# Optimization experiments

Measured on AMD Instinct MI355X. Metric: run time of the kernel, lower is better.

The kernel has to match this reference:

```python
import jax, jax.numpy as jnp
import numpy as np

B, N, D = 8, 65536, 3
K = 64                 # num_centers
NPOINT = 4096
M = NPOINT // K * 2    # max_neighbors = 128
S = NPOINT // K        # fps samples per group = 64
NITER = 10             # KMeans default Niter


def _sqdist(src, dst):
    # ||s||^2 + ||d||^2 - 2 s.d   (same math as (s-d)^2 sum, GEMM form)
    s2 = (src ** 2).sum(-1)[:, :, None]          # [B,N,1]
    d2 = (dst ** 2).sum(-1)[:, None, :]          # [B,1,K]
    return s2 + d2 - 2.0 * jnp.einsum('bnd,bkd->bnk', src, dst)


def _kmeans(x):
    Bb, Nn, Dd = x.shape
    c = x[:, :K, :]
    bidx = jnp.arange(Bb)[:, None]               # broadcast with cl [B,N]
    for _ in range(NITER):
        cl = jnp.argmin(_sqdist(x, c), axis=2)   # [B,N] cluster codes
        c = jnp.zeros((Bb, K, Dd), x.dtype).at[bidx, cl].add(x)
        ncl = jnp.zeros((Bb, K), x.dtype).at[bidx, cl].add(1.0)
        c = c / ncl[:, :, None]
    return c


def _query_neighbor(x, centers):
    dist = _sqdist(x, centers)                   # [B,N,K]
    negd = -jnp.transpose(dist, (0, 2, 1))       # [B,K,N]
    _, nidx = jax.lax.top_k(negd, M)             # M nearest points per center
    bidx = jnp.arange(x.shape[0])[:, None, None]
    return x[bidx, nidx]                         # [B,K,M,3]


def _batch_fps(xyz, farthest0):
    # xyz: [B,G,Nn,3]; sequential farthest-point sampling per group
    Bb, G, Nn, _ = xyz.shape
    dist0 = jnp.full((Bb, G, Nn), 1e10, xyz.dtype)

    def step(carry, _):
        distance, farthest = carry
        centroid = jnp.take_along_axis(xyz, farthest[:, :, None, None], axis=2)  # [B,G,1,3]
        d = ((xyz - centroid) ** 2).sum(-1)       # [B,G,Nn]
        distance = jnp.minimum(distance, d)
        new_far = jnp.argmax(distance, -1).astype(farthest.dtype)
        return (distance, new_far), farthest      # store index BEFORE update

    _, idx = jax.lax.scan(step, (dist0, farthest0), None, length=S)
    idx = jnp.transpose(idx, (1, 2, 0))           # [B,G,S]
    idx3 = jnp.broadcast_to(idx[..., None], idx.shape + (3,))
    new_xyz = jnp.take_along_axis(xyz, idx3, axis=2)  # [B,G,S,3]
    return new_xyz.reshape(Bb, G * S, 3)


def setup_inputs() -> dict:
    key = jax.random.key(0)
    k1, k2 = jax.random.split(key)
    x = jax.random.normal(k1, (B, N, D), dtype=jnp.float32)
    farthest0 = jax.random.randint(k2, (B, K), 0, M, dtype=jnp.int32)
    return {"x": x, "farthest0": farthest0}


def reference(x, farthest0):
    centers = _kmeans(x)                  # [B,K,3]
    neighbor = _query_neighbor(x, centers)  # [B,K,M,3]
    new_xyz = _batch_fps(neighbor, farthest0)  # [B, NPOINT, 3]
    return new_xyz, centers
```

## Files before the change

### kernel.cpp

```cpp
#include <hip/hip_runtime.h>
#include <stdint.h>

#pragma clang fp contract(off)

#define B 8
#define N 65536
#define KC 64
#define M 128
#define S 64
#define NITER 10
#define TOPK_T 1024
#define NWAVES (TOPK_T / 64)
#define HPAD 257
#define SAMPLE 8192
#define SCAP 2048
#define CAP 2048
#define UPD_T 1024
#define RANGE 16384
#define NRANGE (N / RANGE)
#define PPT (RANGE / UPD_T)
#define GBATCH 2048

using u32 = unsigned int;
using u64 = unsigned long long;

__device__ __forceinline__ float sq3(float a, float b, float c) {
  return __fadd_rn(__fadd_rn(__fmul_rn(a, a), __fmul_rn(b, b)), __fmul_rn(c, c));
}
__device__ __forceinline__ float dot3(float x0, float x1, float x2,
                                      float c0, float c1, float c2) {
  return __fadd_rn(__fadd_rn(__fmul_rn(x0, c0), __fmul_rn(x1, c1)), __fmul_rn(x2, c2));
}
__device__ __forceinline__ float distf(float s2, float d2, float dt) {
  return __fsub_rn(__fadd_rn(s2, d2), __fmul_rn(2.0f, dt));
}
__device__ __forceinline__ u32 fkey(float f) {
  u32 u = __float_as_uint(f);
  return (u & 0x80000000u) ? ~u : (u | 0x80000000u);
}


__global__ void k_init_centers(const float* __restrict__ x, float* __restrict__ centers) {
  int i = blockIdx.x * blockDim.x + threadIdx.x;
  if (i >= B * KC * 3) return;
  int b = i / (KC * 3);
  int r = i % (KC * 3);
  centers[i] = x[(size_t)b * N * 3 + r];
}

__global__ void k_s2(const float* __restrict__ x, float* __restrict__ s2) {
  int i = blockIdx.x * blockDim.x + threadIdx.x;
  const float2* x2 = (const float2*)x;
  float2 A = x2[3 * i], Bv = x2[3 * i + 1], C = x2[3 * i + 2];
  float2 o;
  o.x = sq3(A.x, A.y, Bv.x);
  o.y = sq3(Bv.y, C.x, C.y);
  ((float2*)s2)[i] = o;
}

__global__ void k_assign(const float* __restrict__ x, const float* __restrict__ centers,
                         unsigned char* __restrict__ cl) {
  __shared__ float4 cs[KC];
  int g = blockIdx.x;
  int b = g & 7;
  int chunk = g >> 3;
  int t = threadIdx.x;
  if (t < KC) {
    float a0 = centers[(b * KC + t) * 3 + 0];
    float a1 = centers[(b * KC + t) * 3 + 1];
    float a2 = centers[(b * KC + t) * 3 + 2];
    cs[t] = make_float4(a0, a1, a2, sq3(a0, a1, a2));
  }
  __syncthreads();
  int pr = chunk * 256 + t;
  const float2* xb2 = (const float2*)(x + (size_t)b * N * 3);
  float2 A = xb2[3 * pr], Bv = xb2[3 * pr + 1], C = xb2[3 * pr + 2];
  float s20 = sq3(A.x, A.y, Bv.x);
  float s21 = sq3(Bv.y, C.x, C.y);
  float best0 = __int_as_float(0x7f800000), best1 = best0;
  int bi0 = 0, bi1 = 0;
  for (int k = 0; k < KC; ++k) {
    float4 cc = cs[k];
    float d0 = distf(s20, cc.w, dot3(A.x, A.y, Bv.x, cc.x, cc.y, cc.z));
    float d1 = distf(s21, cc.w, dot3(Bv.y, C.x, C.y, cc.x, cc.y, cc.z));
    if (d0 < best0) { best0 = d0; bi0 = k; }
    if (d1 < best1) { best1 = d1; bi1 = k; }
  }
  *(unsigned short*)(cl + (size_t)b * N + 2 * pr) =
      (unsigned short)(bi0 | (bi1 << 8));
}

__global__ __launch_bounds__(UPD_T)
void k_cluster_update(const float* __restrict__ x, const unsigned char* __restrict__ cl,
                      float* __restrict__ centers) {
  __shared__ unsigned short midx[RANGE];
  __shared__ float bcoord[3][GBATCH + 1];
  __shared__ int woff[NWAVES];
  __shared__ int sCnt;
  int g = blockIdx.x;
  int bk = ((g & 7) << 6) | (g >> 3);
  int b = bk >> 6, k = bk & 63;
  int t = threadIdx.x, lane = t & 63, wid = t >> 6;
  const unsigned char* clb = cl + (size_t)b * N;
  const float* xb = x + (size_t)b * N * 3;
  float acc = 0.f;
  int cntAll = 0;

  for (int r = 0; r < NRANGE; ++r) {
    const uint4* cp = (const uint4*)(clb + r * RANGE);
    uint4 v = cp[t];
    u32 wsv[4] = {v.x, v.y, v.z, v.w};
    int m = 0;
#pragma unroll
    for (int j = 0; j < PPT; ++j)
      m += (((wsv[j >> 2] >> ((j & 3) * 8)) & 255u) == (u32)k);
    int incl = m;
#pragma unroll
    for (int o = 1; o < 64; o <<= 1) {
      int u = __shfl_up(incl, o);
      if (lane >= o) incl += u;
    }
    if (lane == 63) woff[wid] = incl;
    __syncthreads();
    if (t == 0) {
      int run = 0;
      for (int w = 0; w < NWAVES; ++w) { int vv = woff[w]; woff[w] = run; run += vv; }
      sCnt = run;
    }
    __syncthreads();
    int off = woff[wid] + incl - m;
    int mcnt = sCnt;
    int base = t * PPT;
#pragma unroll
    for (int j = 0; j < PPT; ++j) {
      if (((wsv[j >> 2] >> ((j & 3) * 8)) & 255u) == (u32)k)
        midx[off++] = (unsigned short)(base + j);
    }
    __syncthreads();
    for (int bo = 0; bo < mcnt; bo += GBATCH) {
      int bn = min(GBATCH, mcnt - bo);
      for (int i = t; i < bn; i += UPD_T) {
        int li = midx[bo + i];
        size_t src = ((size_t)(r * RANGE + li)) * 3;
        bcoord[0][i] = xb[src];
        bcoord[1][i] = xb[src + 1];
        bcoord[2][i] = xb[src + 2];
      }
      __syncthreads();
      if (wid == 0 && lane < 3) {
        const float* mb = &bcoord[lane][0];
        for (int i = 0; i < bn; ++i) acc = __fadd_rn(acc, mb[i]);
      }
      __syncthreads();
    }
    cntAll += mcnt;
    __syncthreads();
  }
  if (wid == 0 && lane < 3)
    centers[bk * 3 + lane] = __fdiv_rn(acc, (float)cntAll);
}

__global__ __launch_bounds__(TOPK_T)
void k_query_topk(const float* __restrict__ x, const float* __restrict__ s2g,
                  const float* __restrict__ centers, float* __restrict__ neighbor) {
  __shared__ u32 whist[NWAVES * HPAD];
  __shared__ u32 hist[256];
  __shared__ u32 skeys[SCAP];
  __shared__ u64 candList[CAP];
  __shared__ u64 lessList[M];
  __shared__ u32 eqList[256];
  __shared__ u32 sPrefix;
  __shared__ int sNeed, sCntBin;
  __shared__ int cntCand, cntLess, cntEq;
  __shared__ float sc0, sc1, sc2, sd2;

  int g = blockIdx.x;
  int bk = ((g & 7) << 6) | (g >> 3);
  int b = bk >> 6;
  int t = threadIdx.x;
  int wid = t >> 6;
  if (t == 0) {
    float c0 = centers[bk * 3], c1 = centers[bk * 3 + 1], c2 = centers[bk * 3 + 2];
    sc0 = c0; sc1 = c1; sc2 = c2; sd2 = sq3(c0, c1, c2);
    cntCand = 0; cntLess = 0; cntEq = 0;
  }
  for (int i = t; i < NWAVES * HPAD; i += TOPK_T) whist[i] = 0;
  __syncthreads();
  float c0 = sc0, c1 = sc1, c2 = sc2, d2 = sd2;
  const float* xb = x + (size_t)b * N * 3;
  const float2* xb2 = (const float2*)xb;
  const float2* s2b2 = (const float2*)(s2g + (size_t)b * N);

  for (int p = t; p < SAMPLE / 2; p += TOPK_T) {
    float2 A = xb2[3 * p], Bv = xb2[3 * p + 1], C = xb2[3 * p + 2];
    float2 s2p = s2b2[p];
    float d0 = distf(s2p.x, d2, dot3(A.x, A.y, Bv.x, c0, c1, c2));
    float d1 = distf(s2p.y, d2, dot3(Bv.y, C.x, C.y, c0, c1, c2));
    atomicAdd(&whist[wid * HPAD + (fkey(d0) >> 24)], 1u);
    atomicAdd(&whist[wid * HPAD + (fkey(d1) >> 24)], 1u);
  }
  __syncthreads();
  if (t < 256) {
    u32 s = 0;
#pragma unroll
    for (int w = 0; w < NWAVES; ++w) s += whist[w * HPAD + t];
    hist[t] = s;
  }
  __syncthreads();
  if (t == 0) {
    int cum = 0;
    for (int bin = 0; bin < 256; ++bin) {
      int c = (int)hist[bin];
      if (cum + c >= M) { sPrefix = (u32)bin; sNeed = M - cum; sCntBin = c; break; }
      cum += c;
    }
  }
  __syncthreads();
  u32 selByte = sPrefix;
  int needEq = sNeed;
  int cntBin = sCntBin;

  u32 thrK;
  if (cntBin <= SCAP) {
    for (int p = t; p < SAMPLE / 2; p += TOPK_T) {
      float2 A = xb2[3 * p], Bv = xb2[3 * p + 1], C = xb2[3 * p + 2];
      float2 s2p = s2b2[p];
      float d0 = distf(s2p.x, d2, dot3(A.x, A.y, Bv.x, c0, c1, c2));
      float d1 = distf(s2p.y, d2, dot3(Bv.y, C.x, C.y, c0, c1, c2));
      u32 k0 = fkey(d0), k1 = fkey(d1);
      if ((k0 >> 24) == selByte) skeys[atomicAdd(&cntEq, 1)] = k0;
      if ((k1 >> 24) == selByte) skeys[atomicAdd(&cntEq, 1)] = k1;
    }
    __syncthreads();
    int ne = cntEq;
    u32 prefix = selByte << 24;
    int need = needEq;
    for (int sh = 16; sh >= 0; sh -= 8) {
      for (int i = t; i < 256; i += TOPK_T) hist[i] = 0;
      __syncthreads();
      for (int i = t; i < ne; i += TOPK_T) {
        u32 kk = skeys[i];
        if ((kk >> (sh + 8)) == (prefix >> (sh + 8)))
          atomicAdd(&hist[(kk >> sh) & 255u], 1u);
      }
      __syncthreads();
      if (t == 0) {
        int cum = 0;
        for (int bin = 0; bin < 256; ++bin) {
          int c = (int)hist[bin];
          if (cum + c >= need) { sPrefix = prefix | ((u32)bin << sh); sNeed = need - cum; break; }
          cum += c;
        }
      }
      __syncthreads();
      prefix = sPrefix; need = sNeed;
      __syncthreads();
    }
    thrK = prefix;
  } else {
    thrK = (selByte << 24) | 0x00FFFFFFu;
  }

  for (int p = t; p < N / 2; p += TOPK_T) {
    float2 A = xb2[3 * p], Bv = xb2[3 * p + 1], C = xb2[3 * p + 2];
    float2 s2p = s2b2[p];
    float d0 = distf(s2p.x, d2, dot3(A.x, A.y, Bv.x, c0, c1, c2));
    float d1 = distf(s2p.y, d2, dot3(Bv.y, C.x, C.y, c0, c1, c2));
    u32 k0 = fkey(d0), k1 = fkey(d1);
    if (k0 <= thrK) {
      int q = atomicAdd(&cntCand, 1);
      if (q < CAP) candList[q] = ((u64)k0 << 32) | (u32)(2 * p);
    }
    if (k1 <= thrK) {
      int q = atomicAdd(&cntCand, 1);
      if (q < CAP) candList[q] = ((u64)k1 << 32) | (u32)(2 * p + 1);
    }
  }
  __syncthreads();
  int cc = cntCand;

  if (cc <= CAP) {
    int P = 1; while (P < cc) P <<= 1;
    if (P < M) P = M;
    for (int i = t; i < P; i += TOPK_T) if (i >= cc) candList[i] = ~0ull;
    __syncthreads();
    for (int ksz = 2; ksz <= P; ksz <<= 1) {
      for (int j = ksz >> 1; j > 0; j >>= 1) {
        for (int idx = t; idx < P; idx += TOPK_T) {
          int ixj = idx ^ j;
          if (ixj > idx) {
            u64 a = candList[idx], bb = candList[ixj];
            bool up = ((idx & ksz) == 0);
            if (up ? (a > bb) : (a < bb)) { candList[idx] = bb; candList[ixj] = a; }
          }
        }
        __syncthreads();
      }
    }
    if (t < M) {
      int idx = (int)(candList[t] & 0xFFFFFFFFu);
      size_t src = ((size_t)b * N + idx) * 3;
      size_t dst = ((size_t)bk * M + t) * 3;
      neighbor[dst]     = x[src];
      neighbor[dst + 1] = x[src + 1];
      neighbor[dst + 2] = x[src + 2];
    }
    return;
  }

  u32 prefix = 0;
  int need = M;
  for (int r = 3; r >= 0; --r) {
    for (int i = t; i < 256; i += TOPK_T) hist[i] = 0;
    __syncthreads();
    int sh = r * 8;
    for (int n = t; n < N; n += TOPK_T) {
      float x0 = xb[n * 3], x1 = xb[n * 3 + 1], x2 = xb[n * 3 + 2];
      float d = distf(sq3(x0, x1, x2), d2, dot3(x0, x1, x2, c0, c1, c2));
      u32 key = fkey(d);
      bool ok = (r == 3) || ((key >> (sh + 8)) == (prefix >> (sh + 8)));
      if (ok) atomicAdd(&hist[(key >> sh) & 255u], 1u);
    }
    __syncthreads();
    if (t == 0) {
      int cum = 0;
      for (int bin = 0; bin < 256; ++bin) {
        int c = (int)hist[bin];
        if (cum + c >= need) { sPrefix = prefix | ((u32)bin << sh); sNeed = need - cum; break; }
        cum += c;
      }
    }
    __syncthreads();
    prefix = sPrefix; need = sNeed;
    __syncthreads();
  }
  u32 K128 = prefix;

  if (t == 0) { cntLess = 0; cntEq = 0; }
  __syncthreads();
  for (int n = t; n < N; n += TOPK_T) {
    float x0 = xb[n * 3], x1 = xb[n * 3 + 1], x2 = xb[n * 3 + 2];
    float d = distf(sq3(x0, x1, x2), d2, dot3(x0, x1, x2, c0, c1, c2));
    u32 key = fkey(d);
    if (key < K128) {
      int p = atomicAdd(&cntLess, 1);
      if (p < M) lessList[p] = ((u64)key << 32) | (u32)n;
    } else if (key == K128) {
      int p = atomicAdd(&cntEq, 1);
      if (p < 256) eqList[p] = (u32)n;
    }
  }
  __syncthreads();
  int nl = cntLess;
  int ne2 = cntEq;
  for (int i = t; i < M; i += TOPK_T) if (i >= nl) lessList[i] = ~0ull;
  for (int i = t; i < 256; i += TOPK_T) if (i >= ne2) eqList[i] = 0xFFFFFFFFu;
  __syncthreads();

  for (int ksz = 2; ksz <= M; ksz <<= 1) {
    for (int j = ksz >> 1; j > 0; j >>= 1) {
      for (int idx = t; idx < M; idx += TOPK_T) {
        int ixj = idx ^ j;
        if (ixj > idx) {
          u64 a = lessList[idx], bb = lessList[ixj];
          bool up = ((idx & ksz) == 0);
          if (up ? (a > bb) : (a < bb)) { lessList[idx] = bb; lessList[ixj] = a; }
        }
      }
      __syncthreads();
    }
  }
  for (int ksz = 2; ksz <= 256; ksz <<= 1) {
    for (int j = ksz >> 1; j > 0; j >>= 1) {
      for (int idx = t; idx < 256; idx += TOPK_T) {
        int ixj = idx ^ j;
        if (ixj > idx) {
          u32 a = eqList[idx], bb = eqList[ixj];
          bool up = ((idx & ksz) == 0);
          if (up ? (a > bb) : (a < bb)) { eqList[idx] = bb; eqList[ixj] = a; }
        }
      }
      __syncthreads();
    }
  }

  if (t < M) {
    int idx = (t < nl) ? (int)(lessList[t] & 0xFFFFFFFFu) : (int)eqList[t - nl];
    size_t src = ((size_t)b * N + idx) * 3;
    size_t dst = ((size_t)bk * M + t) * 3;
    neighbor[dst]     = x[src];
    neighbor[dst + 1] = x[src + 1];
    neighbor[dst + 2] = x[src + 2];
  }
}

__global__ void k_fps(const float* __restrict__ neighbor, const int* __restrict__ farthest0,
                      const float* __restrict__ centers, float* __restrict__ out) {
  __shared__ float px[M], py[M], pz[M];
  __shared__ float wv[2];
  __shared__ int wi[2];
  int bg = blockIdx.x;
  int b = bg >> 6, g = bg & 63;
  int t = threadIdx.x;
  {
    int i = bg * 128 + t;
    if (i < B * KC * 3) out[B * 4096 * 3 + i] = centers[i];
  }
  size_t src = ((size_t)bg * M + t) * 3;
  float mx = neighbor[src], my = neighbor[src + 1], mz = neighbor[src + 2];
  px[t] = mx; py[t] = my; pz[t] = mz;
  int far = farthest0[bg];
  float dist = 1e10f;
  __syncthreads();
  for (int s = 0; s < S; ++s) {
    if (t == far) {
      size_t dst = ((size_t)b * 4096 + g * 64 + s) * 3;
      out[dst] = mx; out[dst + 1] = my; out[dst + 2] = mz;
    }
    float cx = px[far], cy = py[far], cz = pz[far];
    float dx = __fsub_rn(mx, cx), dy = __fsub_rn(my, cy), dz = __fsub_rn(mz, cz);
    float d = sq3(dx, dy, dz);
    dist = fminf(dist, d);
    float v = dist;
    int i = t;
#pragma unroll
    for (int off = 1; off < 64; off <<= 1) {
      float ov = __shfl_xor(v, off);
      int oi = __shfl_xor(i, off);
      if (ov > v || (ov == v && oi < i)) { v = ov; i = oi; }
    }
    int wid = t >> 6;
    if ((t & 63) == 0) { wv[wid] = v; wi[wid] = i; }
    __syncthreads();
    float v0 = wv[0]; int i0 = wi[0];
    float v1 = wv[1]; int i1 = wi[1];
    far = (v1 > v0 || (v1 == v0 && i1 < i0)) ? i1 : i0;
    __syncthreads();
  }
}

extern "C" void kernel_launch(void* const* d_in, const int* in_sizes, int n_in,
                              void* d_out, int out_size, void* d_ws, size_t ws_size,
                              hipStream_t stream) {
  const float* x = (const float*)d_in[0];
  const int* farthest0 = (const int*)d_in[1];
  float* out = (float*)d_out;

  char* w = (char*)d_ws;
  float* centers         = (float*)(w);
  unsigned char* cl      = (unsigned char*)(w + 8192);
  float* s2              = (float*)(w + 8192 + 524288);
  float* neighbor        = (float*)(w + 8192 + 524288 + 2097152);

  k_init_centers<<<6, 256, 0, stream>>>(x, centers);
  k_s2<<<B * N / 2 / 256, 256, 0, stream>>>(x, s2);
  for (int it = 0; it < NITER; ++it) {
    k_assign<<<B * 128, 256, 0, stream>>>(x, centers, cl);
    k_cluster_update<<<B * KC, UPD_T, 0, stream>>>(x, cl, centers);
  }
  k_query_topk<<<B * KC, TOPK_T, 0, stream>>>(x, s2, centers, neighbor);
  k_fps<<<B * KC, M, 0, stream>>>(neighbor, farthest0, centers, out);
}
```

Measured before the change: 552.4 us.

## Split top-k query into threshold, point-parallel scatter, and per-center sort kernels

Replaces the monolithic per-center top-k kernel with three stages. A small kernel estimates a coarse threshold per center from a sample. A point-parallel kernel reads each point once, tests it against all 64 centers and appends candidate indices to global per-center lists. A final kernel recomputes distances for the candidates and sorts them. This removes the per-center full scans of all N points, which meant each batch's points were read 64 times, and drops the s2 precompute kernel. In exchange it adds global atomics, a coarser threshold that produces more candidates to sort, and a global candidate buffer with a fallback path when a list overflows.

```diff
diff --git a/kernel.cpp b/kernel.cpp
--- a/kernel.cpp
+++ b/kernel.cpp
@@ -9,12 +9,11 @@
 #define M 128
 #define S 64
 #define NITER 10
-#define TOPK_T 1024
-#define NWAVES (TOPK_T / 64)
+#define NWAVES 16
 #define HPAD 257
 #define SAMPLE 8192
-#define SCAP 2048
-#define CAP 2048
+#define CAPG 3072
+#define TCAP 4096
 #define UPD_T 1024
 #define RANGE 16384
 #define NRANGE (N / RANGE)
@@ -46,16 +45,6 @@
   int b = i / (KC * 3);
   int r = i % (KC * 3);
   centers[i] = x[(size_t)b * N * 3 + r];
-}
-
-__global__ void k_s2(const float* __restrict__ x, float* __restrict__ s2) {
-  int i = blockIdx.x * blockDim.x + threadIdx.x;
-  const float2* x2 = (const float2*)x;
-  float2 A = x2[3 * i], Bv = x2[3 * i + 1], C = x2[3 * i + 2];
-  float2 o;
-  o.x = sq3(A.x, A.y, Bv.x);
-  o.y = sq3(Bv.y, C.x, C.y);
-  ((float2*)s2)[i] = o;
 }
 
 __global__ void k_assign(const float* __restrict__ x, const float* __restrict__ centers,
@@ -160,133 +149,132 @@
     centers[bk * 3 + lane] = __fdiv_rn(acc, (float)cntAll);
 }
 
-__global__ __launch_bounds__(TOPK_T)
-void k_query_topk(const float* __restrict__ x, const float* __restrict__ s2g,
-                  const float* __restrict__ centers, float* __restrict__ neighbor) {
-  __shared__ u32 whist[NWAVES * HPAD];
+__global__ __launch_bounds__(256)
+void k_thresh(const float* __restrict__ x, const float* __restrict__ centers,
+              u32* __restrict__ thr, u32* __restrict__ cnt) {
+  __shared__ u32 whist[4 * HPAD];
+  __shared__ int sv[256];
+  __shared__ float4 scen;
+  int g = blockIdx.x;
+  int bk = ((g & 7) << 6) | (g >> 3);
+  int b = bk >> 6;
+  int t = threadIdx.x, wid = t >> 6;
+  if (t == 0) {
+    float c0 = centers[bk * 3], c1 = centers[bk * 3 + 1], c2 = centers[bk * 3 + 2];
+    scen = make_float4(c0, c1, c2, sq3(c0, c1, c2));
+    cnt[bk] = 0;
+  }
+  for (int i = t; i < 4 * HPAD; i += 256) whist[i] = 0;
+  __syncthreads();
+  float c0 = scen.x, c1 = scen.y, c2 = scen.z, d2 = scen.w;
+  const float2* xb2 = (const float2*)(x + (size_t)b * N * 3);
+  for (int p = t; p < SAMPLE / 2; p += 256) {
+    float2 A = xb2[3 * p], Bv = xb2[3 * p + 1], C = xb2[3 * p + 2];
+    float s20 = sq3(A.x, A.y, Bv.x);
+    float s21 = sq3(Bv.y, C.x, C.y);
+    float d0 = distf(s20, d2, dot3(A.x, A.y, Bv.x, c0, c1, c2));
+    float d1 = distf(s21, d2, dot3(Bv.y, C.x, C.y, c0, c1, c2));
+    atomicAdd(&whist[wid * HPAD + (fkey(d0) >> 24)], 1u);
+    atomicAdd(&whist[wid * HPAD + (fkey(d1) >> 24)], 1u);
+  }
+  __syncthreads();
+  int own = (int)(whist[0 * HPAD + t] + whist[1 * HPAD + t] +
+                  whist[2 * HPAD + t] + whist[3 * HPAD + t]);
+  sv[t] = own;
+  __syncthreads();
+  for (int off = 1; off < 256; off <<= 1) {
+    int add = (t >= off) ? sv[t - off] : 0;
+    __syncthreads();
+    sv[t] += add;
+    __syncthreads();
+  }
+  if (sv[t] >= M && sv[t] - own < M)
+    thr[bk] = ((u32)t << 24) | 0x00FFFFFFu;
+}
+
+__global__ void k_scatter_test(const float* __restrict__ x, const float* __restrict__ centers,
+                               const u32* __restrict__ thr, u32* __restrict__ cnt,
+                               u32* __restrict__ cand) {
+  __shared__ float4 cs[KC];
+  __shared__ u32 lthr[KC];
+  int g = blockIdx.x;
+  int b = g & 7;
+  int chunk = g >> 3;
+  int t = threadIdx.x;
+  if (t < KC) {
+    float a0 = centers[(b * KC + t) * 3 + 0];
+    float a1 = centers[(b * KC + t) * 3 + 1];
+    float a2 = centers[(b * KC + t) * 3 + 2];
+    cs[t] = make_float4(a0, a1, a2, sq3(a0, a1, a2));
+    lthr[t] = thr[b * KC + t];
+  }
+  __syncthreads();
+  int pr = chunk * 256 + t;
+  const float2* xb2 = (const float2*)(x + (size_t)b * N * 3);
+  float2 A = xb2[3 * pr], Bv = xb2[3 * pr + 1], C = xb2[3 * pr + 2];
+  float s20 = sq3(A.x, A.y, Bv.x);
+  float s21 = sq3(Bv.y, C.x, C.y);
+  u32 n0 = 2 * pr, n1 = 2 * pr + 1;
+  for (int k = 0; k < KC; ++k) {
+    float4 cc = cs[k];
+    float d0 = distf(s20, cc.w, dot3(A.x, A.y, Bv.x, cc.x, cc.y, cc.z));
+    float d1 = distf(s21, cc.w, dot3(Bv.y, C.x, C.y, cc.x, cc.y, cc.z));
+    u32 k0 = fkey(d0), k1 = fkey(d1);
+    int bkk = b * KC + k;
+    if (k0 <= lthr[k]) {
+      u32 p = atomicAdd(&cnt[bkk], 1u);
+      if (p < CAPG) cand[(size_t)bkk * CAPG + p] = n0;
+    }
+    if (k1 <= lthr[k]) {
+      u32 p = atomicAdd(&cnt[bkk], 1u);
+      if (p < CAPG) cand[(size_t)bkk * CAPG + p] = n1;
+    }
+  }
+}
+
+__global__ __launch_bounds__(1024)
+void k_topk_sort(const float* __restrict__ x, const float* __restrict__ centers,
+                 const u32* __restrict__ cnt, const u32* __restrict__ cand,
+                 float* __restrict__ neighbor) {
+  __shared__ u64 candList[TCAP];
   __shared__ u32 hist[256];
-  __shared__ u32 skeys[SCAP];
-  __shared__ u64 candList[CAP];
   __shared__ u64 lessList[M];
   __shared__ u32 eqList[256];
   __shared__ u32 sPrefix;
-  __shared__ int sNeed, sCntBin;
-  __shared__ int cntCand, cntLess, cntEq;
-  __shared__ float sc0, sc1, sc2, sd2;
-
+  __shared__ int sNeed;
+  __shared__ int cntLess, cntEq;
+  __shared__ float4 scen;
   int g = blockIdx.x;
   int bk = ((g & 7) << 6) | (g >> 3);
   int b = bk >> 6;
   int t = threadIdx.x;
-  int wid = t >> 6;
   if (t == 0) {
     float c0 = centers[bk * 3], c1 = centers[bk * 3 + 1], c2 = centers[bk * 3 + 2];
-    sc0 = c0; sc1 = c1; sc2 = c2; sd2 = sq3(c0, c1, c2);
-    cntCand = 0; cntLess = 0; cntEq = 0;
-  }
-  for (int i = t; i < NWAVES * HPAD; i += TOPK_T) whist[i] = 0;
-  __syncthreads();
-  float c0 = sc0, c1 = sc1, c2 = sc2, d2 = sd2;
+    scen = make_float4(c0, c1, c2, sq3(c0, c1, c2));
+    cntLess = 0; cntEq = 0;
+  }
+  __syncthreads();
+  float c0 = scen.x, c1 = scen.y, c2 = scen.z, d2 = scen.w;
   const float* xb = x + (size_t)b * N * 3;
-  const float2* xb2 = (const float2*)xb;
-  const float2* s2b2 = (const float2*)(s2g + (size_t)b * N);
-
-  for (int p = t; p < SAMPLE / 2; p += TOPK_T) {
-    float2 A = xb2[3 * p], Bv = xb2[3 * p + 1], C = xb2[3 * p + 2];
-    float2 s2p = s2b2[p];
-    float d0 = distf(s2p.x, d2, dot3(A.x, A.y, Bv.x, c0, c1, c2));
-    float d1 = distf(s2p.y, d2, dot3(Bv.y, C.x, C.y, c0, c1, c2));
-    atomicAdd(&whist[wid * HPAD + (fkey(d0) >> 24)], 1u);
-    atomicAdd(&whist[wid * HPAD + (fkey(d1) >> 24)], 1u);
-  }
-  __syncthreads();
-  if (t < 256) {
-    u32 s = 0;
-#pragma unroll
-    for (int w = 0; w < NWAVES; ++w) s += whist[w * HPAD + t];
-    hist[t] = s;
-  }
-  __syncthreads();
-  if (t == 0) {
-    int cum = 0;
-    for (int bin = 0; bin < 256; ++bin) {
-      int c = (int)hist[bin];
-      if (cum + c >= M) { sPrefix = (u32)bin; sNeed = M - cum; sCntBin = c; break; }
-      cum += c;
-    }
-  }
-  __syncthreads();
-  u32 selByte = sPrefix;
-  int needEq = sNeed;
-  int cntBin = sCntBin;
-
-  u32 thrK;
-  if (cntBin <= SCAP) {
-    for (int p = t; p < SAMPLE / 2; p += TOPK_T) {
-      float2 A = xb2[3 * p], Bv = xb2[3 * p + 1], C = xb2[3 * p + 2];
-      float2 s2p = s2b2[p];
-      float d0 = distf(s2p.x, d2, dot3(A.x, A.y, Bv.x, c0, c1, c2));
-      float d1 = distf(s2p.y, d2, dot3(Bv.y, C.x, C.y, c0, c1, c2));
-      u32 k0 = fkey(d0), k1 = fkey(d1);
-      if ((k0 >> 24) == selByte) skeys[atomicAdd(&cntEq, 1)] = k0;
-      if ((k1 >> 24) == selByte) skeys[atomicAdd(&cntEq, 1)] = k1;
-    }
-    __syncthreads();
-    int ne = cntEq;
-    u32 prefix = selByte << 24;
-    int need = needEq;
-    for (int sh = 16; sh >= 0; sh -= 8) {
-      for (int i = t; i < 256; i += TOPK_T) hist[i] = 0;
-      __syncthreads();
-      for (int i = t; i < ne; i += TOPK_T) {
-        u32 kk = skeys[i];
-        if ((kk >> (sh + 8)) == (prefix >> (sh + 8)))
-          atomicAdd(&hist[(kk >> sh) & 255u], 1u);
-      }
-      __syncthreads();
-      if (t == 0) {
-        int cum = 0;
-        for (int bin = 0; bin < 256; ++bin) {
-          int c = (int)hist[bin];
-          if (cum + c >= need) { sPrefix = prefix | ((u32)bin << sh); sNeed = need - cum; break; }
-          cum += c;
-        }
-      }
-      __syncthreads();
-      prefix = sPrefix; need = sNeed;
-      __syncthreads();
-    }
-    thrK = prefix;
-  } else {
-    thrK = (selByte << 24) | 0x00FFFFFFu;
-  }
-
-  for (int p = t; p < N / 2; p += TOPK_T) {
-    float2 A = xb2[3 * p], Bv = xb2[3 * p + 1], C = xb2[3 * p + 2];
-    float2 s2p = s2b2[p];
-    float d0 = distf(s2p.x, d2, dot3(A.x, A.y, Bv.x, c0, c1, c2));
-    float d1 = distf(s2p.y, d2, dot3(Bv.y, C.x, C.y, c0, c1, c2));
-    u32 k0 = fkey(d0), k1 = fkey(d1);
-    if (k0 <= thrK) {
-      int q = atomicAdd(&cntCand, 1);
-      if (q < CAP) candList[q] = ((u64)k0 << 32) | (u32)(2 * p);
-    }
-    if (k1 <= thrK) {
-      int q = atomicAdd(&cntCand, 1);
-      if (q < CAP) candList[q] = ((u64)k1 << 32) | (u32)(2 * p + 1);
-    }
-  }
-  __syncthreads();
-  int cc = cntCand;
-
-  if (cc <= CAP) {
-    int P = 1; while (P < cc) P <<= 1;
-    if (P < M) P = M;
-    for (int i = t; i < P; i += TOPK_T) if (i >= cc) candList[i] = ~0ull;
+  int cc = (int)cnt[bk];
+
+  if (cc <= CAPG) {
+    const u32* cb = cand + (size_t)bk * CAPG;
+    int P = M; while (P < cc) P <<= 1;
+    for (int i = t; i < P; i += 1024) {
+      if (i < cc) {
+        u32 n = cb[i];
+        float x0 = xb[n * 3], x1 = xb[n * 3 + 1], x2 = xb[n * 3 + 2];
+        float d = distf(sq3(x0, x1, x2), d2, dot3(x0, x1, x2, c0, c1, c2));
+        candList[i] = ((u64)fkey(d) << 32) | n;
+      } else {
+        candList[i] = ~0ull;
+      }
+    }
     __syncthreads();
     for (int ksz = 2; ksz <= P; ksz <<= 1) {
       for (int j = ksz >> 1; j > 0; j >>= 1) {
-        for (int idx = t; idx < P; idx += TOPK_T) {
+        for (int idx = t; idx < P; idx += 1024) {
           int ixj = idx ^ j;
           if (ixj > idx) {
             u64 a = candList[idx], bb = candList[ixj];
@@ -311,10 +299,10 @@
   u32 prefix = 0;
   int need = M;
   for (int r = 3; r >= 0; --r) {
-    for (int i = t; i < 256; i += TOPK_T) hist[i] = 0;
+    for (int i = t; i < 256; i += 1024) hist[i] = 0;
     __syncthreads();
     int sh = r * 8;
-    for (int n = t; n < N; n += TOPK_T) {
+    for (int n = t; n < N; n += 1024) {
       float x0 = xb[n * 3], x1 = xb[n * 3 + 1], x2 = xb[n * 3 + 2];
       float d = distf(sq3(x0, x1, x2), d2, dot3(x0, x1, x2, c0, c1, c2));
       u32 key = fkey(d);
@@ -338,7 +326,7 @@
 
   if (t == 0) { cntLess = 0; cntEq = 0; }
   __syncthreads();
-  for (int n = t; n < N; n += TOPK_T) {
+  for (int n = t; n < N; n += 1024) {
     float x0 = xb[n * 3], x1 = xb[n * 3 + 1], x2 = xb[n * 3 + 2];
     float d = distf(sq3(x0, x1, x2), d2, dot3(x0, x1, x2, c0, c1, c2));
     u32 key = fkey(d);
@@ -353,13 +341,13 @@
   __syncthreads();
   int nl = cntLess;
   int ne2 = cntEq;
-  for (int i = t; i < M; i += TOPK_T) if (i >= nl) lessList[i] = ~0ull;
-  for (int i = t; i < 256; i += TOPK_T) if (i >= ne2) eqList[i] = 0xFFFFFFFFu;
+  for (int i = t; i < M; i += 1024) if (i >= nl) lessList[i] = ~0ull;
+  for (int i = t; i < 256; i += 1024) if (i >= ne2) eqList[i] = 0xFFFFFFFFu;
   __syncthreads();
 
   for (int ksz = 2; ksz <= M; ksz <<= 1) {
     for (int j = ksz >> 1; j > 0; j >>= 1) {
-      for (int idx = t; idx < M; idx += TOPK_T) {
+      for (int idx = t; idx < M; idx += 1024) {
         int ixj = idx ^ j;
         if (ixj > idx) {
           u64 a = lessList[idx], bb = lessList[ixj];
@@ -372,7 +360,7 @@
   }
   for (int ksz = 2; ksz <= 256; ksz <<= 1) {
     for (int j = ksz >> 1; j > 0; j >>= 1) {
-      for (int idx = t; idx < 256; idx += TOPK_T) {
+      for (int idx = t; idx < 256; idx += 1024) {
         int ixj = idx ^ j;
         if (ixj > idx) {
           u32 a = eqList[idx], bb = eqList[ixj];
@@ -449,15 +437,18 @@
   char* w = (char*)d_ws;
   float* centers         = (float*)(w);
   unsigned char* cl      = (unsigned char*)(w + 8192);
-  float* s2              = (float*)(w + 8192 + 524288);
-  float* neighbor        = (float*)(w + 8192 + 524288 + 2097152);
+  u32* thr               = (u32*)(w + 8192 + 524288);
+  u32* cnt               = (u32*)(w + 8192 + 524288 + 2048);
+  float* neighbor        = (float*)(w + 8192 + 524288 + 4096);
+  u32* cand              = (u32*)(w + 8192 + 524288 + 4096 + 786432);
 
   k_init_centers<<<6, 256, 0, stream>>>(x, centers);
-  k_s2<<<B * N / 2 / 256, 256, 0, stream>>>(x, s2);
   for (int it = 0; it < NITER; ++it) {
     k_assign<<<B * 128, 256, 0, stream>>>(x, centers, cl);
     k_cluster_update<<<B * KC, UPD_T, 0, stream>>>(x, cl, centers);
   }
-  k_query_topk<<<B * KC, TOPK_T, 0, stream>>>(x, s2, centers, neighbor);
+  k_thresh<<<B * KC, 256, 0, stream>>>(x, centers, thr, cnt);
+  k_scatter_test<<<B * 128, 256, 0, stream>>>(x, centers, thr, cnt, cand);
+  k_topk_sort<<<B * KC, 1024, 0, stream>>>(x, centers, cnt, cand, neighbor);
   k_fps<<<B * KC, M, 0, stream>>>(neighbor, farthest0, centers, out);
 }
```

Measured after the change: 1.531 ms. +177.2%, slower.
